# Performance work log

Hardware: AMD Instinct MI355X
Metric: run time of the kernel (lower is better)

The kernel has to match this reference:

```python
import jax, jax.numpy as jnp
import numpy as np

DIM = 1024
HEADS = 16
HEAD_DIM = 64
INNER = HEADS * HEAD_DIM


def setup_inputs() -> dict:
    key = jax.random.key(0)
    ks = jax.random.split(key, 6)
    x = jax.random.normal(ks[0], (4, 2048, DIM), dtype=jnp.float32)
    # torch nn.Linear weight shape [out, in]; store as [in, out] for x @ W
    Wq = jax.random.normal(ks[1], (DIM, INNER), dtype=jnp.float32) * (DIM ** -0.5)
    Wk = jax.random.normal(ks[2], (DIM, INNER), dtype=jnp.float32) * (DIM ** -0.5)
    Wv = jax.random.normal(ks[3], (DIM, INNER), dtype=jnp.float32) * (DIM ** -0.5)
    Wo = jax.random.normal(ks[4], (INNER, DIM), dtype=jnp.float32) * (INNER ** -0.5)
    bo = jax.random.normal(ks[5], (DIM,), dtype=jnp.float32) * 0.01
    return {"x": x, "Wq": Wq, "Wk": Wk, "Wv": Wv, "Wo": Wo, "bo": bo}


def reference(x, Wq, Wk, Wv, Wo, bo):
    b, n, _ = x.shape
    # projections, split heads: [b, n, inner] -> [b, h, n, d]
    split = lambda t: t.reshape(b, n, HEADS, HEAD_DIM).transpose(0, 2, 1, 3)
    q = split(x @ Wq)
    k = split(x @ Wk)
    v = split(x @ Wv)
    scale = HEAD_DIM ** -0.5
    sim = jnp.einsum('bhnd,bhmd->bhnm', q, k) * scale
    attn = jax.nn.softmax(sim, axis=-1)
    out = jnp.einsum('bhnm,bhmd->bhnd', attn, v)
    out = out.transpose(0, 2, 1, 3).reshape(b, n, INNER)
    return out @ Wo + bo
```

## Files before the change

### kernel.cpp

```cpp
#include <hip/hip_runtime.h>
#include <hip/hip_bf16.h>
#include <stdint.h>

typedef unsigned short u16;
typedef __bf16 bf16x8_t __attribute__((ext_vector_type(8)));
typedef float f32x4_t __attribute__((ext_vector_type(4)));
typedef float f32x16_t __attribute__((ext_vector_type(16)));
typedef unsigned int u32x2_t __attribute__((ext_vector_type(2)));

__device__ __forceinline__ u16 f2bf(float f) {
    union { float f; uint32_t u; } c; c.f = f;
    uint32_t r = c.u + 0x7FFFu + ((c.u >> 16) & 1u);
    return (u16)(r >> 16);
}

__device__ __forceinline__ uint32_t pk2(float a, float b) {
    union { __bf16 h[2]; uint32_t u; } z;
    z.h[0] = (__bf16)a; z.h[1] = (__bf16)b;
    return z.u;
}

__device__ __forceinline__ void gld_lds16(const void* g, void* l) {
    __builtin_amdgcn_global_load_lds(
        (__attribute__((address_space(1))) void*)(g),
        (__attribute__((address_space(3))) void*)(l), 16, 0, 0);
}

#define QSCALE 0.18033688011112042f

__global__ void k_convert_x(const float* __restrict__ x, u16* __restrict__ xb) {
    int i = blockIdx.x * 256 + threadIdx.x;
    float4 v = ((const float4*)x)[i];
    ushort4 o;
    o.x = f2bf(v.x); o.y = f2bf(v.y); o.z = f2bf(v.z); o.w = f2bf(v.w);
    ((ushort4*)xb)[i] = o;
}

__global__ void k_convert_wT(const float* __restrict__ w0, const float* __restrict__ w1,
                             const float* __restrict__ w2, const float* __restrict__ w3,
                             u16* __restrict__ wT) {
    __shared__ u16 t[32][33];
    const float* src = (blockIdx.z == 0) ? w0 : (blockIdx.z == 1) ? w1 : (blockIdx.z == 2) ? w2 : w3;
    u16* dst = wT + (size_t)blockIdx.z * (1024 * 1024);
    int n0 = blockIdx.x * 32, k0 = blockIdx.y * 32;
    int tx = threadIdx.x & 31, ty = threadIdx.x >> 5;
    #pragma unroll
    for (int r = 0; r < 4; ++r) {
        int kl = ty * 4 + r;
        t[tx][kl] = f2bf(src[(size_t)(k0 + kl) * 1024 + n0 + tx]);
    }
    __syncthreads();
    #pragma unroll
    for (int r = 0; r < 4; ++r) {
        int nl = ty * 4 + r;
        dst[(size_t)(n0 + nl) * 1024 + k0 + tx] = t[nl][tx];
    }
}

template <int MODE>
__global__ __launch_bounds__(256, 2) void k_gemm(
    const u16* __restrict__ A, const u16* __restrict__ WT,
    const float* __restrict__ bias,
    u16* __restrict__ qo, u16* __restrict__ ko, u16* __restrict__ vt,
    float* __restrict__ out) {
    __shared__ u16 lA[128 * 64];
    __shared__ u16 lB[128 * 64];
    const int tid = threadIdx.x, wv = tid >> 6, ln = tid & 63;
    const int lo = ln & 15, jg = ln >> 4;
    const int m0 = blockIdx.x * 128;
    int mat, n0;
    if (MODE == 0) { mat = blockIdx.y >> 3; n0 = (blockIdx.y & 7) * 128; }
    else           { mat = 3;               n0 = blockIdx.y * 128; }
    const u16* Bt = WT + (size_t)mat * (1024 * 1024);
    const int wm = wv >> 1, wn = wv & 1;

    f32x4_t acc[4][4];
    #pragma unroll
    for (int i = 0; i < 4; ++i)
        #pragma unroll
        for (int j = 0; j < 4; ++j) acc[i][j] = (f32x4_t){0.f, 0.f, 0.f, 0.f};

    for (int k0 = 0; k0 < 1024; k0 += 64) {
        __syncthreads();
        #pragma unroll
        for (int is = 0; is < 4; ++is) {
            int c = is * 256 + tid;
            int r = c >> 3;
            int j = (c & 7) ^ (r & 7);
            gld_lds16(A  + (size_t)(m0 + r) * 1024 + k0 + j * 8, &lA[(is * 256 + wv * 64) * 8]);
            gld_lds16(Bt + (size_t)(n0 + r) * 1024 + k0 + j * 8, &lB[(is * 256 + wv * 64) * 8]);
        }
        __syncthreads();
        #pragma unroll
        for (int sub = 0; sub < 2; ++sub) {
            bf16x8_t af[4], bfr[4];
            #pragma unroll
            for (int i = 0; i < 4; ++i) {
                int r = wm * 64 + i * 16 + lo;
                af[i] = *(const bf16x8_t*)&lA[(r * 8 + ((sub * 4 + jg) ^ (r & 7))) * 8];
            }
            #pragma unroll
            for (int j = 0; j < 4; ++j) {
                int r = wn * 64 + j * 16 + lo;
                bfr[j] = *(const bf16x8_t*)&lB[(r * 8 + ((sub * 4 + jg) ^ (r & 7))) * 8];
            }
            #pragma unroll
            for (int i = 0; i < 4; ++i)
                #pragma unroll
                for (int j = 0; j < 4; ++j)
                    acc[i][j] = __builtin_amdgcn_mfma_f32_16x16x32_bf16(af[i], bfr[j], acc[i][j], 0, 0, 0);
        }
    }

    if (MODE == 0) {
        if (mat == 2) {
            #pragma unroll
            for (int j = 0; j < 4; ++j) {
                int col = n0 + wn * 64 + j * 16 + lo;
                int hh = col >> 6, dd = col & 63;
                #pragma unroll
                for (int i = 0; i < 4; ++i) {
                    int m = m0 + wm * 64 + i * 16 + jg * 4;
                    int bb = m >> 11, nn = m & 2047;
                    ushort4 pkv;
                    pkv.x = f2bf(acc[i][j][0]);
                    pkv.y = f2bf(acc[i][j][1]);
                    pkv.z = f2bf(acc[i][j][2]);
                    pkv.w = f2bf(acc[i][j][3]);
                    *(ushort4*)&vt[(((size_t)(bb * 16 + hh)) * 64 + dd) * 2048 + nn] = pkv;
                }
            }
        } else {
            u16* dst = (mat == 0) ? qo : ko;
            float sc = (mat == 0) ? QSCALE : 1.0f;
            #pragma unroll
            for (int j = 0; j < 4; ++j) {
                int col = n0 + wn * 64 + j * 16 + lo;
                int hh = col >> 6, dd = col & 63;
                #pragma unroll
                for (int i = 0; i < 4; ++i)
                    #pragma unroll
                    for (int rg = 0; rg < 4; ++rg) {
                        int m = m0 + wm * 64 + i * 16 + jg * 4 + rg;
                        int bb = m >> 11, nn = m & 2047;
                        dst[(((size_t)(bb * 16 + hh)) * 2048 + nn) * 64 + dd] = f2bf(acc[i][j][rg] * sc);
                    }
            }
        }
    } else {
        #pragma unroll
        for (int j = 0; j < 4; ++j) {
            int col = n0 + wn * 64 + j * 16 + lo;
            float bv = bias[col];
            #pragma unroll
            for (int i = 0; i < 4; ++i)
                #pragma unroll
                for (int rg = 0; rg < 4; ++rg) {
                    int m = m0 + wm * 64 + i * 16 + jg * 4 + rg;
                    out[(size_t)m * 1024 + col] = acc[i][j][rg] + bv;
                }
        }
    }
}

__global__ __launch_bounds__(512, 4) void k_attn(
    const u16* __restrict__ Q, const u16* __restrict__ K,
    const u16* __restrict__ Vg, u16* __restrict__ ctx) {
    __shared__ __align__(16) u16 Kl[2][64 * 64];
    __shared__ __align__(16) u16 Vt[2][64 * 64];

    const int tid = threadIdx.x, wv = tid >> 6, ln = tid & 63;
    const int lq = ln & 31, hi = ln >> 5;
    const int bh = blockIdx.x;
    const int b = bh >> 4, h = bh & 15;
    const size_t base = (size_t)bh * 2048 * 64;
    const u16* Vtg = Vg + (size_t)bh * 64 * 2048;
    const int q0 = blockIdx.y * 256 + wv * 32;

    bf16x8_t bQ[4];
    {
        const u16* qp = Q + base + (size_t)(q0 + lq) * 64 + hi * 8;
        #pragma unroll
        for (int s = 0; s < 4; ++s) bQ[s] = *(const bf16x8_t*)(qp + s * 16);
    }
    bf16x8_t ones;
    #pragma unroll
    for (int e = 0; e < 8; ++e) ones[e] = (__bf16)1.0f;
    f32x16_t zro;
    #pragma unroll
    for (int e = 0; e < 16; ++e) zro[e] = 0.f;

    f32x16_t acc[2], lacc;
    #pragma unroll
    for (int e = 0; e < 16; ++e) { acc[0][e] = 0.f; acc[1][e] = 0.f; lacc[e] = 0.f; }

    auto stageK = [&](int buf, int kv0) {
        int r = tid >> 3;
        int j = (tid & 7) ^ (r & 7);
        gld_lds16(K + base + (size_t)(kv0 + r) * 64 + j * 8, &Kl[buf][wv * 64 * 8]);
    };
    auto stageV = [&](int buf, int kv0) {
        int r = tid >> 3;
        int j = (tid & 7) ^ (r & 7);
        gld_lds16(Vtg + (size_t)r * 2048 + kv0 + j * 8, &Vt[buf][wv * 64 * 8]);
    };

    const int swl = lq & 7;

    auto compute = [&](int c) {
        f32x16_t z0, z1;
        {
            const bf16x8_t aK = *(const bf16x8_t*)&Kl[c][lq * 64 + ((hi ^ swl) * 8)];
            z0 = __builtin_amdgcn_mfma_f32_32x32x16_bf16(aK, bQ[0], zro, 0, 0, 0);
        }
        #pragma unroll
        for (int s = 1; s < 4; ++s) {
            const bf16x8_t aK = *(const bf16x8_t*)
                &Kl[c][lq * 64 + (((2 * s + hi) ^ swl) * 8)];
            z0 = __builtin_amdgcn_mfma_f32_32x32x16_bf16(aK, bQ[s], z0, 0, 0, 0);
        }
        {
            const bf16x8_t aK = *(const bf16x8_t*)&Kl[c][(32 + lq) * 64 + ((hi ^ swl) * 8)];
            z1 = __builtin_amdgcn_mfma_f32_32x32x16_bf16(aK, bQ[0], zro, 0, 0, 0);
        }
        #pragma unroll
        for (int s = 1; s < 4; ++s) {
            const bf16x8_t aK = *(const bf16x8_t*)
                &Kl[c][(32 + lq) * 64 + (((2 * s + hi) ^ swl) * 8)];
            z1 = __builtin_amdgcn_mfma_f32_32x32x16_bf16(aK, bQ[s], z1, 0, 0, 0);
        }
        #pragma unroll
        for (int kg = 0; kg < 2; ++kg) {
            const f32x16_t& z = kg ? z1 : z0;
            uint32_t w[4][2];
            #pragma unroll
            for (int m = 0; m < 4; ++m) {
                float p0 = __builtin_amdgcn_exp2f(z[4 * m + 0]);
                float p1 = __builtin_amdgcn_exp2f(z[4 * m + 1]);
                float p2 = __builtin_amdgcn_exp2f(z[4 * m + 2]);
                float p3 = __builtin_amdgcn_exp2f(z[4 * m + 3]);
                w[m][0] = pk2(p0, p1);
                w[m][1] = pk2(p2, p3);
            }
            #pragma unroll
            for (int sl = 0; sl < 2; ++sl) {
                const int ma = 2 * sl, sp = 2 * kg + sl;
                u32x2_t r0 = __builtin_amdgcn_permlane32_swap(w[ma][0], w[ma + 1][0], false, false);
                u32x2_t r1 = __builtin_amdgcn_permlane32_swap(w[ma][1], w[ma + 1][1], false, false);
                union { uint32_t u[4]; bf16x8_t v; } ap;
                ap.u[0] = r0[0]; ap.u[1] = r1[0]; ap.u[2] = r0[1]; ap.u[3] = r1[1];
                lacc = __builtin_amdgcn_mfma_f32_32x32x16_bf16(ap.v, ones, lacc, 0, 0, 0);
                #pragma unroll
                for (int dh = 0; dh < 2; ++dh) {
                    const bf16x8_t bV = *(const bf16x8_t*)
                        &Vt[c][(dh * 32 + lq) * 64 + (((2 * sp + hi) ^ swl) * 8)];
                    acc[dh] = __builtin_amdgcn_mfma_f32_32x32x16_bf16(ap.v, bV, acc[dh], 0, 0, 0);
                }
            }
        }
    };

    stageK(0, 0);
    stageV(0, 0);
    __syncthreads();

    for (int i = 0; i < 16; ++i) {
        const int t = 2 * i;
        stageK(1, (t + 1) * 64);
        stageV(1, (t + 1) * 64);
        compute(0);
        __syncthreads();
        if (t + 2 < 32) {
            stageK(0, (t + 2) * 64);
            stageV(0, (t + 2) * 64);
        }
        compute(1);
        __syncthreads();
    }

    f32x16_t linv;
    #pragma unroll
    for (int e = 0; e < 16; ++e) linv[e] = 1.0f / lacc[e];
    #pragma unroll
    for (int dh = 0; dh < 2; ++dh) {
        int d = dh * 32 + lq;
        #pragma unroll
        for (int e = 0; e < 16; ++e) {
            int q = q0 + (e & 3) + 8 * (e >> 2) + 4 * hi;
            ctx[((size_t)(b * 2048 + q)) * 1024 + h * 64 + d] = f2bf(acc[dh][e] * linv[e]);
        }
    }
}

extern "C" void kernel_launch(void* const* d_in, const int* in_sizes, int n_in,
                              void* d_out, int out_size, void* d_ws, size_t ws_size,
                              hipStream_t stream) {
    const float* x  = (const float*)d_in[0];
    const float* Wq = (const float*)d_in[1];
    const float* Wk = (const float*)d_in[2];
    const float* Wv = (const float*)d_in[3];
    const float* Wo = (const float*)d_in[4];
    const float* bo = (const float*)d_in[5];
    float* out = (float*)d_out;

    char* ws = (char*)d_ws;
    u16* xb   = (u16*)(ws);
    u16* wT   = (u16*)(ws + 16777216);
    u16* qb   = (u16*)(ws + 25165824);
    u16* kb   = (u16*)(ws + 41943040);
    u16* vtb  = (u16*)(ws + 58720256);
    u16* ctx  = (u16*)(ws + 75497472);

    k_convert_x<<<8192, 256, 0, stream>>>(x, xb);
    k_convert_wT<<<dim3(32, 32, 4), 256, 0, stream>>>(Wq, Wk, Wv, Wo, wT);
    k_gemm<0><<<dim3(64, 24), 256, 0, stream>>>(xb, wT, nullptr, qb, kb, vtb, nullptr);
    k_attn<<<dim3(64, 8), 512, 0, stream>>>(qb, kb, vtb, ctx);
    k_gemm<1><<<dim3(64, 8), 256, 0, stream>>>(ctx, wT, bo, nullptr, nullptr, nullptr, out);
}
```

Measured before the change: 172.8 us.

## Software-pipeline QK^T one tile ahead of softmax-PV with triple-buffered V

Splits the attention inner loop into a QK^T stage and an exp/PV stage and runs QK^T for tile t+1 while exp and PV run for tile t. K stays double buffered and V becomes triple buffered so loads can run two tiles ahead. The block shrinks from 512 to 256 threads (128 queries per block), which doubles the grid and has each thread stage two 16-byte chunks per tile. The goal is to overlap MFMA work with exp/transcendental work and memory latency. The cost is more live registers for the second score set and a lower declared occupancy in the launch bounds.

```diff
diff --git a/kernel.cpp b/kernel.cpp
--- a/kernel.cpp
+++ b/kernel.cpp
@@ -163,11 +163,11 @@
     }
 }
 
-__global__ __launch_bounds__(512, 4) void k_attn(
+__global__ __launch_bounds__(256, 3) void k_attn(
     const u16* __restrict__ Q, const u16* __restrict__ K,
     const u16* __restrict__ Vg, u16* __restrict__ ctx) {
-    __shared__ __align__(16) u16 Kl[2][64 * 64];
-    __shared__ __align__(16) u16 Vt[2][64 * 64];
+    __shared__ __align__(16) u16 Kl[2 * 64 * 64];
+    __shared__ __align__(16) u16 Vl[3 * 64 * 64];
 
     const int tid = threadIdx.x, wv = tid >> 6, ln = tid & 63;
     const int lq = ln & 31, hi = ln >> 5;
@@ -175,7 +175,7 @@
     const int b = bh >> 4, h = bh & 15;
     const size_t base = (size_t)bh * 2048 * 64;
     const u16* Vtg = Vg + (size_t)bh * 64 * 2048;
-    const int q0 = blockIdx.y * 256 + wv * 32;
+    const int q0 = blockIdx.y * 128 + wv * 32;
 
     bf16x8_t bQ[4];
     {
@@ -194,41 +194,57 @@
     #pragma unroll
     for (int e = 0; e < 16; ++e) { acc[0][e] = 0.f; acc[1][e] = 0.f; lacc[e] = 0.f; }
 
-    auto stageK = [&](int buf, int kv0) {
-        int r = tid >> 3;
-        int j = (tid & 7) ^ (r & 7);
-        gld_lds16(K + base + (size_t)(kv0 + r) * 64 + j * 8, &Kl[buf][wv * 64 * 8]);
+    auto stageK = [&](int tt) {
+        if (tt >= 32) return;
+        u16* dst = &Kl[(tt & 1) * 4096];
+        #pragma unroll
+        for (int is = 0; is < 2; ++is) {
+            int c = is * 256 + tid;
+            int r = c >> 3;
+            int j = (c & 7) ^ (r & 7);
+            gld_lds16(K + base + (size_t)(tt * 64 + r) * 64 + j * 8,
+                      dst + (is * 256 + wv * 64) * 8);
+        }
     };
-    auto stageV = [&](int buf, int kv0) {
-        int r = tid >> 3;
-        int j = (tid & 7) ^ (r & 7);
-        gld_lds16(Vtg + (size_t)r * 2048 + kv0 + j * 8, &Vt[buf][wv * 64 * 8]);
+    auto stageV = [&](int tt) {
+        if (tt >= 32) return;
+        u16* dst = &Vl[(tt % 3) * 4096];
+        #pragma unroll
+        for (int is = 0; is < 2; ++is) {
+            int c = is * 256 + tid;
+            int r = c >> 3;
+            int j = (c & 7) ^ (r & 7);
+            gld_lds16(Vtg + (size_t)r * 2048 + tt * 64 + j * 8,
+                      dst + (is * 256 + wv * 64) * 8);
+        }
     };
 
     const int swl = lq & 7;
 
-    auto compute = [&](int c) {
-        f32x16_t z0, z1;
+    auto QKc = [&](int tt, f32x16_t& z0, f32x16_t& z1) {
+        const u16* Kb = &Kl[(tt & 1) * 4096];
         {
-            const bf16x8_t aK = *(const bf16x8_t*)&Kl[c][lq * 64 + ((hi ^ swl) * 8)];
+            const bf16x8_t aK = *(const bf16x8_t*)&Kb[lq * 64 + ((hi ^ swl) * 8)];
             z0 = __builtin_amdgcn_mfma_f32_32x32x16_bf16(aK, bQ[0], zro, 0, 0, 0);
         }
         #pragma unroll
         for (int s = 1; s < 4; ++s) {
-            const bf16x8_t aK = *(const bf16x8_t*)
-                &Kl[c][lq * 64 + (((2 * s + hi) ^ swl) * 8)];
+            const bf16x8_t aK = *(const bf16x8_t*)&Kb[lq * 64 + (((2 * s + hi) ^ swl) * 8)];
             z0 = __builtin_amdgcn_mfma_f32_32x32x16_bf16(aK, bQ[s], z0, 0, 0, 0);
         }
         {
-            const bf16x8_t aK = *(const bf16x8_t*)&Kl[c][(32 + lq) * 64 + ((hi ^ swl) * 8)];
+            const bf16x8_t aK = *(const bf16x8_t*)&Kb[(32 + lq) * 64 + ((hi ^ swl) * 8)];
             z1 = __builtin_amdgcn_mfma_f32_32x32x16_bf16(aK, bQ[0], zro, 0, 0, 0);
         }
         #pragma unroll
         for (int s = 1; s < 4; ++s) {
-            const bf16x8_t aK = *(const bf16x8_t*)
-                &Kl[c][(32 + lq) * 64 + (((2 * s + hi) ^ swl) * 8)];
+            const bf16x8_t aK = *(const bf16x8_t*)&Kb[(32 + lq) * 64 + (((2 * s + hi) ^ swl) * 8)];
             z1 = __builtin_amdgcn_mfma_f32_32x32x16_bf16(aK, bQ[s], z1, 0, 0, 0);
         }
+    };
+
+    auto EXPPV = [&](int tt, const f32x16_t& z0, const f32x16_t& z1) {
+        const u16* Vb = &Vl[(tt % 3) * 4096];
         #pragma unroll
         for (int kg = 0; kg < 2; ++kg) {
             const f32x16_t& z = kg ? z1 : z0;
@@ -253,29 +269,30 @@
                 #pragma unroll
                 for (int dh = 0; dh < 2; ++dh) {
                     const bf16x8_t bV = *(const bf16x8_t*)
-                        &Vt[c][(dh * 32 + lq) * 64 + (((2 * sp + hi) ^ swl) * 8)];
+                        &Vb[(dh * 32 + lq) * 64 + (((2 * sp + hi) ^ swl) * 8)];
                     acc[dh] = __builtin_amdgcn_mfma_f32_32x32x16_bf16(ap.v, bV, acc[dh], 0, 0, 0);
                 }
             }
         }
     };
 
-    stageK(0, 0);
-    stageV(0, 0);
+    f32x16_t zA0, zA1, zB0, zB1;
+
+    stageK(0); stageV(0);
     __syncthreads();
+    stageK(1); stageV(1);
+    QKc(0, zA0, zA1);
 
     for (int i = 0; i < 16; ++i) {
         const int t = 2 * i;
-        stageK(1, (t + 1) * 64);
-        stageV(1, (t + 1) * 64);
-        compute(0);
         __syncthreads();
-        if (t + 2 < 32) {
-            stageK(0, (t + 2) * 64);
-            stageV(0, (t + 2) * 64);
-        }
-        compute(1);
+        stageK(t + 2); stageV(t + 2);
+        QKc(t + 1, zB0, zB1);
+        EXPPV(t, zA0, zA1);
         __syncthreads();
+        stageK(t + 3); stageV(t + 3);
+        if (i < 15) QKc(t + 2, zA0, zA1);
+        EXPPV(t + 1, zB0, zB1);
     }
 
     f32x16_t linv;
@@ -314,6 +331,6 @@
     k_convert_x<<<8192, 256, 0, stream>>>(x, xb);
     k_convert_wT<<<dim3(32, 32, 4), 256, 0, stream>>>(Wq, Wk, Wv, Wo, wT);
     k_gemm<0><<<dim3(64, 24), 256, 0, stream>>>(xb, wT, nullptr, qb, kb, vtb, nullptr);
-    k_attn<<<dim3(64, 8), 512, 0, stream>>>(qb, kb, vtb, ctx);
+    k_attn<<<dim3(64, 16), 256, 0, stream>>>(qb, kb, vtb, ctx);
     k_gemm<1><<<dim3(64, 8), 256, 0, stream>>>(ctx, wT, bo, nullptr, nullptr, nullptr, out);
 }
```

Result: slower. 182.5 us (+5.6%).
